# Optimization experiments

Measured on AMD Instinct MI355X. Metric: run time of the kernel, lower is better.

## Reference

```python
import jax, jax.numpy as jnp
import numpy as np

B, T, S, D = 16, 64, 256, 512
NEG_INF = -1e9  # finite stand-in for -inf mask fill (identical sparsemax output, autodiff-safe)


def sparsemax(z, axis=-1):
    # sparsemax(z) = clip(z - tau, 0), tau from sorted cumsum threshold
    z = z - jnp.max(z, axis=axis, keepdims=True)
    z_srt = -jnp.sort(-z, axis=axis)                      # descending sort
    z_cum = jnp.cumsum(z_srt, axis=axis) - 1.0
    k = jnp.arange(1, z.shape[axis] + 1, dtype=z.dtype)   # rho = 1..d
    support = (k * z_srt) > z_cum
    supp_size = jnp.sum(support, axis=axis, keepdims=True)
    tau = jnp.take_along_axis(z_cum, supp_size - 1, axis=axis) / supp_size.astype(z.dtype)
    return jnp.clip(z - tau, 0.0)


def setup_inputs() -> dict:
    key = jax.random.key(0)
    ks = jax.random.split(key, 9)
    init = lambda k, shape: (jax.random.normal(k, shape, jnp.float32) * 0.05)
    return {
        "source": jax.random.normal(ks[0], (B, T, D), jnp.float32),
        "memory_bank": jax.random.normal(ks[1], (B, S, D), jnp.float32),
        "memory_mask": jax.random.randint(ks[2], (B, S), 0, 2).astype(jnp.int32),
        "W_q": init(ks[3], (D, D)),   # linear_query weight
        "b_q": init(ks[4], (D,)),     # linear_query bias
        "W_c": init(ks[5], (D, D)),   # linear_context weight (no bias)
        "v": init(ks[6], (D,)),       # v projection (dim -> 1)
        "W_out": init(ks[7], (D, 2 * D)),  # linear_out weight
        "b_out": init(ks[8], (D,)),        # linear_out bias (mlp path has bias)
    }


def reference(source, memory_bank, memory_mask, W_q, b_q, W_c, v, W_out, b_out):
    # MLP (Bahdanau) score: v^T tanh(W_q q + U_c h)
    wq = jnp.einsum('btd,ed->bte', source, W_q) + b_q        # (B,T,D)
    uh = jnp.einsum('bsd,ed->bse', memory_bank, W_c)         # (B,S,D)
    wquh = jnp.tanh(wq[:, :, None, :] + uh[:, None, :, :])   # (B,T,S,D) big intermediate
    align = jnp.einsum('btsd,d->bts', wquh, v)               # (B,T,S)
    align = jnp.where(memory_mask[:, None, :].astype(bool), align, NEG_INF)
    align_vectors = sparsemax(align, axis=-1)                # (B,T,S)
    c = jnp.einsum('bts,bsd->btd', align_vectors, memory_bank)
    concat_c = jnp.concatenate([c, source], axis=-1)         # (B,T,2D)
    attn_h = jnp.einsum('btf,df->btd', concat_c, W_out) + b_out  # no tanh on mlp path
    return attn_h.transpose(1, 0, 2), align_vectors.transpose(1, 0, 2)
```

## Files before the change

kernel.cpp:

```cpp
#include <hip/hip_runtime.h>
#include <hip/hip_bf16.h>

#define BB 16
#define TT 64
#define SS 256
#define DD 512

typedef __bf16 bf16x8 __attribute__((ext_vector_type(8)));
typedef float f32x4 __attribute__((ext_vector_type(4)));

__device__ __forceinline__ ushort f2b(float x) {
    __hip_bfloat16 h = __float2bfloat16(x);
    return __builtin_bit_cast(ushort, h);
}
__device__ __forceinline__ float b2f(ushort u) {
    unsigned int x = (unsigned int)u << 16;
    return __builtin_bit_cast(float, x);
}

#define S_SRC (BB * TT * DD)
#define S_MB  (BB * SS * DD)
#define S_WQ  (DD * DD)
#define S_WC  (DD * DD)
#define S_WO  (DD * 2 * DD)

__global__ __launch_bounds__(256) void cast_all(
    const float* __restrict__ src, const float* __restrict__ mb,
    const float* __restrict__ wq, const float* __restrict__ wc,
    const float* __restrict__ wo,
    ushort* __restrict__ src_b, ushort* __restrict__ mb_b,
    ushort* __restrict__ wq_b, ushort* __restrict__ wc_b,
    ushort* __restrict__ wo_b) {
    int g = blockIdx.x * 256 + threadIdx.x;
    const int G0 = S_SRC / 4, G1 = S_MB / 4, G2 = S_WQ / 4, G3 = S_WC / 4;
    const float* in;
    ushort* out;
    int local;
    if (g < G0) { in = src; out = src_b; local = g; }
    else if (g < G0 + G1) { in = mb; out = mb_b; local = g - G0; }
    else if (g < G0 + G1 + G2) { in = wq; out = wq_b; local = g - G0 - G1; }
    else if (g < G0 + G1 + G2 + G3) { in = wc; out = wc_b; local = g - G0 - G1 - G2; }
    else { in = wo; out = wo_b; local = g - G0 - G1 - G2 - G3; }
    float4 x = *(const float4*)(in + (size_t)local * 4);
    ushort4 y = {f2b(x.x), f2b(x.y), f2b(x.z), f2b(x.w)};
    *(ushort4*)(out + (size_t)local * 4) = y;
}

__global__ __launch_bounds__(256) void mega_gemm(
    const ushort* __restrict__ src_b, const ushort* __restrict__ mb_b,
    const ushort* __restrict__ wqw_b, const ushort* __restrict__ wcw_b,
    const ushort* __restrict__ wo_b,
    const float* __restrict__ b_q, const float* __restrict__ b_out,
    float* __restrict__ Ewq, float* __restrict__ Y,
    ushort* __restrict__ EuT, ushort* __restrict__ M2) {
    __shared__ ushort Asm[64 * 72];
    __shared__ ushort Bsm[64 * 72];
    const int id = blockIdx.x;
    const ushort* Ab;
    const ushort* Bb;
    const float* bias = nullptr;
    void* Cp;
    int ldb, N, m0, n0;
    bool exp2x, obf16, hasb;
    size_t coff = 0;
    if (id < 256) {
        const bool isY = id >= 128;
        const int l = id & 127;
        m0 = (l >> 3) * 64; n0 = (l & 7) * 64;
        Ab = src_b;
        Bb = isY ? (wo_b + DD) : wqw_b;
        ldb = isY ? 2 * DD : DD;
        bias = isY ? b_out : b_q;
        hasb = true; exp2x = !isY; obf16 = false; N = DD;
        Cp = isY ? (void*)Y : (void*)Ewq;
    } else if (id < 768) {
        const int l = id - 256;
        const int bz = l >> 5, tl = l & 31;
        m0 = (tl >> 2) * 64; n0 = (tl & 3) * 64;
        Ab = wcw_b;
        Bb = mb_b + (size_t)bz * SS * DD;
        ldb = DD;
        hasb = false; exp2x = true; obf16 = true; N = SS;
        Cp = (void*)EuT; coff = (size_t)bz * DD * SS;
    } else {
        const int l = id - 768;
        const int bz = l >> 5, tl = l & 31;
        m0 = (tl >> 3) * 64; n0 = (tl & 7) * 64;
        Ab = mb_b + (size_t)bz * SS * DD;
        Bb = wo_b;
        ldb = 2 * DD;
        hasb = false; exp2x = false; obf16 = true; N = DD;
        Cp = (void*)M2; coff = (size_t)bz * SS * DD;
    }

    const int tid = threadIdx.x;
    const int lane = tid & 63;
    const int wave = tid >> 6;
    const int wm = wave & 1, wn = wave >> 1;

    const int srow = tid >> 3;
    const int schunk = tid & 7;
    const ushort* Ag0 = Ab + (size_t)(m0 + srow) * DD + schunk * 8;
    const ushort* Ag1 = Ag0 + (size_t)32 * DD;
    const ushort* Bg0 = Bb + (size_t)(n0 + srow) * ldb + schunk * 8;
    const ushort* Bg1 = Bg0 + (size_t)32 * ldb;
    const int lw = srow * 72 + schunk * 8;

    const int l15 = lane & 15, quad = lane >> 4;
    const int ar = (wm * 32 + l15) * 72 + quad * 8;
    const int br = (wn * 32 + l15) * 72 + quad * 8;

    f32x4 acc00 = {0.f, 0.f, 0.f, 0.f}, acc01 = {0.f, 0.f, 0.f, 0.f};
    f32x4 acc10 = {0.f, 0.f, 0.f, 0.f}, acc11 = {0.f, 0.f, 0.f, 0.f};

    uint4 a0 = *(const uint4*)Ag0;
    uint4 a1 = *(const uint4*)Ag1;
    uint4 b0 = *(const uint4*)Bg0;
    uint4 b1 = *(const uint4*)Bg1;
    const int P = DD >> 6;
    for (int p = 0; p < P; ++p) {
        __syncthreads();
        *(uint4*)&Asm[lw] = a0;
        *(uint4*)&Asm[lw + 32 * 72] = a1;
        *(uint4*)&Bsm[lw] = b0;
        *(uint4*)&Bsm[lw + 32 * 72] = b1;
        __syncthreads();
        if (p + 1 < P) {
            int ko = (p + 1) << 6;
            a0 = *(const uint4*)(Ag0 + ko);
            a1 = *(const uint4*)(Ag1 + ko);
            b0 = *(const uint4*)(Bg0 + ko);
            b1 = *(const uint4*)(Bg1 + ko);
        }
        bf16x8 fa0 = *(const bf16x8*)&Asm[ar];
        bf16x8 fa1 = *(const bf16x8*)&Asm[ar + 16 * 72];
        bf16x8 fb0 = *(const bf16x8*)&Bsm[br];
        bf16x8 fb1 = *(const bf16x8*)&Bsm[br + 16 * 72];
        acc00 = __builtin_amdgcn_mfma_f32_16x16x32_bf16(fa0, fb0, acc00, 0, 0, 0);
        acc01 = __builtin_amdgcn_mfma_f32_16x16x32_bf16(fa0, fb1, acc01, 0, 0, 0);
        acc10 = __builtin_amdgcn_mfma_f32_16x16x32_bf16(fa1, fb0, acc10, 0, 0, 0);
        acc11 = __builtin_amdgcn_mfma_f32_16x16x32_bf16(fa1, fb1, acc11, 0, 0, 0);
        fa0 = *(const bf16x8*)&Asm[ar + 32];
        fa1 = *(const bf16x8*)&Asm[ar + 16 * 72 + 32];
        fb0 = *(const bf16x8*)&Bsm[br + 32];
        fb1 = *(const bf16x8*)&Bsm[br + 16 * 72 + 32];
        acc00 = __builtin_amdgcn_mfma_f32_16x16x32_bf16(fa0, fb0, acc00, 0, 0, 0);
        acc01 = __builtin_amdgcn_mfma_f32_16x16x32_bf16(fa0, fb1, acc01, 0, 0, 0);
        acc10 = __builtin_amdgcn_mfma_f32_16x16x32_bf16(fa1, fb0, acc10, 0, 0, 0);
        acc11 = __builtin_amdgcn_mfma_f32_16x16x32_bf16(fa1, fb1, acc11, 0, 0, 0);
    }
    const int nA = n0 + wn * 32 + l15;
    float bias0 = 0.f, bias1 = 0.f;
    if (hasb) { bias0 = bias[nA]; bias1 = bias[nA + 16]; }
    float* Cf = (float*)Cp;
    ushort* Cb = (ushort*)Cp;
#pragma unroll
    for (int mt = 0; mt < 2; ++mt) {
        f32x4 accN0 = mt ? acc10 : acc00;
        f32x4 accN1 = mt ? acc11 : acc01;
#pragma unroll
        for (int r = 0; r < 4; ++r) {
            int m = m0 + wm * 32 + mt * 16 + quad * 4 + r;
            float v0 = accN0[r] + bias0;
            float v1 = accN1[r] + bias1;
            if (exp2x) { v0 = __expf(2.0f * v0); v1 = __expf(2.0f * v1); }
            size_t i0 = coff + (size_t)m * N + nA;
            if (obf16) { Cb[i0] = f2b(v0); Cb[i0 + 16] = f2b(v1); }
            else { Cf[i0] = v0; Cf[i0 + 16] = v1; }
        }
    }
}

__global__ __launch_bounds__(256) void align5(const float* __restrict__ Ewq,
                                              const ushort* __restrict__ EuT,
                                              const int* __restrict__ mask,
                                              const float* __restrict__ v,
                                              const ushort* __restrict__ M2,
                                              const float* __restrict__ Y,
                                              float* __restrict__ align_out,
                                              float* __restrict__ out0) {
    const int tg = blockIdx.x, b = blockIdx.y;
    const int t0 = tg * 2, t1 = t0 + 1;
    const int bt0 = b * TT + t0, bt1 = bt0 + 1;
    const int tid = threadIdx.x;
    const int lane = tid & 63;
    const int wave = tid >> 6;
    __shared__ float4 EL[DD];
    __shared__ float zs0[SS], zs1[SS];
    __shared__ float svp[4];
    __shared__ float4 cmb[2][128];
    __shared__ int lst0[SS], lst1[SS];
    __shared__ int cnt[2];

    if (tid < 2) cnt[tid] = 0;
    const float* E0p = Ewq + (size_t)bt0 * DD;
    const float* E1p = Ewq + (size_t)bt1 * DD;
    float pv = 0.f;
    for (int d = tid; d < DD; d += 256) {
        float vv = v[d];
        EL[d] = make_float4(E0p[d], E1p[d], vv, 0.f);
        pv += vv;
    }
#pragma unroll
    for (int off = 32; off > 0; off >>= 1) pv += __shfl_xor(pv, off, 64);
    if (lane == 0) svp[wave] = pv;
    __syncthreads();
    const float sv = svp[0] + svp[1] + svp[2] + svp[3];

    const ushort* U = EuT + (size_t)b * DD * SS + tid;
    float a0 = 0.f, a1 = 0.f;
#pragma unroll 16
    for (int d = 0; d < DD; ++d) {
        float u = b2f(U[(size_t)d * SS]);
        float4 el = EL[d];
        float den0 = __builtin_fmaf(el.x, u, 1.0f);
        float den1 = __builtin_fmaf(el.y, u, 1.0f);
        a0 = __builtin_fmaf(el.z, __builtin_amdgcn_rcpf(den0), a0);
        a1 = __builtin_fmaf(el.z, __builtin_amdgcn_rcpf(den1), a1);
    }
    int mk = mask[b * SS + tid];
    zs0[tid] = mk ? (sv - 2.0f * a0) : -1e9f;
    zs1[tid] = mk ? (sv - 2.0f * a1) : -1e9f;
    __syncthreads();

    if (wave < 2) {
        float* zz = wave ? zs1 : zs0;
        float z0 = zz[lane];
        float z1 = zz[lane + 64];
        float z2 = zz[lane + 128];
        float z3 = zz[lane + 192];
        float mx = fmaxf(fmaxf(z0, z1), fmaxf(z2, z3));
#pragma unroll
        for (int off = 32; off > 0; off >>= 1) mx = fmaxf(mx, __shfl_xor(mx, off, 64));
        z0 -= mx; z1 -= mx; z2 -= mx; z3 -= mx;
        float lo = -1.0f, hi = 0.0f;
        for (int it = 0; it < 24; ++it) {
            float mid = 0.5f * (lo + hi);
            float ssum = fmaxf(z0 - mid, 0.f) + fmaxf(z1 - mid, 0.f) +
                         fmaxf(z2 - mid, 0.f) + fmaxf(z3 - mid, 0.f);
#pragma unroll
            for (int off = 32; off > 0; off >>= 1) ssum += __shfl_xor(ssum, off, 64);
            if (ssum >= 1.0f) lo = mid; else hi = mid;
        }
        float tau = 0.5f * (lo + hi);
        zz[lane] = fmaxf(z0 - tau, 0.f);
        zz[lane + 64] = fmaxf(z1 - tau, 0.f);
        zz[lane + 128] = fmaxf(z2 - tau, 0.f);
        zz[lane + 192] = fmaxf(z3 - tau, 0.f);
    }
    __syncthreads();

    align_out[((size_t)t0 * BB + b) * SS + tid] = zs0[tid];
    align_out[((size_t)t1 * BB + b) * SS + tid] = zs1[tid];

    if (zs0[tid] > 0.f) lst0[atomicAdd(&cnt[0], 1)] = tid;
    if (zs1[tid] > 0.f) lst1[atomicAdd(&cnt[1], 1)] = tid;
    __syncthreads();
    const int n0c = cnt[0], n1c = cnt[1];

    const int ch = tid & 127, sg = tid >> 7;
    const ushort* M2b = M2 + (size_t)b * SS * DD + ch * 4;
    float4 at0 = {0.f, 0.f, 0.f, 0.f}, at1 = {0.f, 0.f, 0.f, 0.f};
#pragma unroll 4
    for (int j = sg; j < n0c; j += 2) {
        int s = lst0[j];
        float p = zs0[s];
        ushort4 m4 = *(const ushort4*)(M2b + (size_t)s * DD);
        at0.x = __builtin_fmaf(p, b2f(m4.x), at0.x);
        at0.y = __builtin_fmaf(p, b2f(m4.y), at0.y);
        at0.z = __builtin_fmaf(p, b2f(m4.z), at0.z);
        at0.w = __builtin_fmaf(p, b2f(m4.w), at0.w);
    }
#pragma unroll 4
    for (int j = sg; j < n1c; j += 2) {
        int s = lst1[j];
        float p = zs1[s];
        ushort4 m4 = *(const ushort4*)(M2b + (size_t)s * DD);
        at1.x = __builtin_fmaf(p, b2f(m4.x), at1.x);
        at1.y = __builtin_fmaf(p, b2f(m4.y), at1.y);
        at1.z = __builtin_fmaf(p, b2f(m4.z), at1.z);
        at1.w = __builtin_fmaf(p, b2f(m4.w), at1.w);
    }
    if (sg == 1) { cmb[0][ch] = at0; cmb[1][ch] = at1; }
    __syncthreads();
    if (sg == 0) {
        float4 p0 = cmb[0][ch], p1 = cmb[1][ch];
        const float4* Y0 = (const float4*)(Y + (size_t)bt0 * DD);
        const float4* Y1 = (const float4*)(Y + (size_t)bt1 * DD);
        float4 y0 = Y0[ch], y1 = Y1[ch];
        float4 o0, o1;
        o0.x = at0.x + p0.x + y0.x; o0.y = at0.y + p0.y + y0.y;
        o0.z = at0.z + p0.z + y0.z; o0.w = at0.w + p0.w + y0.w;
        o1.x = at1.x + p1.x + y1.x; o1.y = at1.y + p1.y + y1.y;
        o1.z = at1.z + p1.z + y1.z; o1.w = at1.w + p1.w + y1.w;
        float4* O0 = (float4*)(out0 + ((size_t)t0 * BB + b) * DD);
        float4* O1 = (float4*)(out0 + ((size_t)t1 * BB + b) * DD);
        O0[ch] = o0;
        O1[ch] = o1;
    }
}

extern "C" void kernel_launch(void* const* d_in, const int* in_sizes, int n_in,
                              void* d_out, int out_size, void* d_ws, size_t ws_size,
                              hipStream_t stream) {
    const float* source = (const float*)d_in[0];
    const float* memory_bank = (const float*)d_in[1];
    const int* memory_mask = (const int*)d_in[2];
    const float* W_q = (const float*)d_in[3];
    const float* b_q = (const float*)d_in[4];
    const float* W_c = (const float*)d_in[5];
    const float* v = (const float*)d_in[6];
    const float* W_out = (const float*)d_in[7];
    const float* b_out = (const float*)d_in[8];

    float* out0 = (float*)d_out;
    float* out1 = out0 + (size_t)TT * BB * DD;

    float* Ewq = (float*)d_ws;
    float* Y = Ewq + S_SRC;
    ushort* EuT = (ushort*)(Y + S_SRC);
    ushort* M2 = EuT + S_MB;
    ushort* src_b = M2 + S_MB;
    ushort* mb_b = src_b + S_SRC;
    ushort* wqw_b = mb_b + S_MB;
    ushort* wcw_b = wqw_b + S_WQ;
    ushort* wo_b = wcw_b + S_WC;

    dim3 blk(256);
    int ngroups = (S_SRC + S_MB + S_WQ + S_WC + S_WO) / 4;
    cast_all<<<dim3(ngroups / 256), blk, 0, stream>>>(
        source, memory_bank, W_q, W_c, W_out, src_b, mb_b, wqw_b, wcw_b, wo_b);
    mega_gemm<<<dim3(1280), blk, 0, stream>>>(
        src_b, mb_b, wqw_b, wcw_b, wo_b, b_q, b_out, Ewq, Y, EuT, M2);
    align5<<<dim3(TT / 2, BB), blk, 0, stream>>>(
        Ewq, EuT, memory_mask, v, M2, Y, out1, out0);
}
```

Baseline: 125.4 us.

## Fuse fp32-to-bf16 cast into GEMM loads and double-buffer shared memory

Removes the separate cast_all kernel. The GEMM now reads fp32 inputs directly and packs them to bf16 while writing them into shared memory. This drops one launch and the write and re-read of the bf16 copies. The shared-memory tiles are also double-buffered so there is one barrier per k-step instead of two, and the launch bound requests 4 blocks per CU. In exchange, each GEMM tile reads twice the bytes from global memory, and memory_bank and the weights are re-read in fp32 by many blocks. Register pressure also rises from holding eight float4 prefetch registers.

```diff
diff --git a/kernel.cpp b/kernel.cpp
--- a/kernel.cpp
+++ b/kernel.cpp
@@ -17,47 +17,27 @@
     unsigned int x = (unsigned int)u << 16;
     return __builtin_bit_cast(float, x);
 }
-
-#define S_SRC (BB * TT * DD)
-#define S_MB  (BB * SS * DD)
-#define S_WQ  (DD * DD)
-#define S_WC  (DD * DD)
-#define S_WO  (DD * 2 * DD)
-
-__global__ __launch_bounds__(256) void cast_all(
+__device__ __forceinline__ uint4 pack8(float4 lo, float4 hi) {
+    uint4 r;
+    r.x = (unsigned)f2b(lo.x) | ((unsigned)f2b(lo.y) << 16);
+    r.y = (unsigned)f2b(lo.z) | ((unsigned)f2b(lo.w) << 16);
+    r.z = (unsigned)f2b(hi.x) | ((unsigned)f2b(hi.y) << 16);
+    r.w = (unsigned)f2b(hi.z) | ((unsigned)f2b(hi.w) << 16);
+    return r;
+}
+
+__global__ __launch_bounds__(256, 4) void mega_gemm(
     const float* __restrict__ src, const float* __restrict__ mb,
     const float* __restrict__ wq, const float* __restrict__ wc,
     const float* __restrict__ wo,
-    ushort* __restrict__ src_b, ushort* __restrict__ mb_b,
-    ushort* __restrict__ wq_b, ushort* __restrict__ wc_b,
-    ushort* __restrict__ wo_b) {
-    int g = blockIdx.x * 256 + threadIdx.x;
-    const int G0 = S_SRC / 4, G1 = S_MB / 4, G2 = S_WQ / 4, G3 = S_WC / 4;
-    const float* in;
-    ushort* out;
-    int local;
-    if (g < G0) { in = src; out = src_b; local = g; }
-    else if (g < G0 + G1) { in = mb; out = mb_b; local = g - G0; }
-    else if (g < G0 + G1 + G2) { in = wq; out = wq_b; local = g - G0 - G1; }
-    else if (g < G0 + G1 + G2 + G3) { in = wc; out = wc_b; local = g - G0 - G1 - G2; }
-    else { in = wo; out = wo_b; local = g - G0 - G1 - G2 - G3; }
-    float4 x = *(const float4*)(in + (size_t)local * 4);
-    ushort4 y = {f2b(x.x), f2b(x.y), f2b(x.z), f2b(x.w)};
-    *(ushort4*)(out + (size_t)local * 4) = y;
-}
-
-__global__ __launch_bounds__(256) void mega_gemm(
-    const ushort* __restrict__ src_b, const ushort* __restrict__ mb_b,
-    const ushort* __restrict__ wqw_b, const ushort* __restrict__ wcw_b,
-    const ushort* __restrict__ wo_b,
     const float* __restrict__ b_q, const float* __restrict__ b_out,
     float* __restrict__ Ewq, float* __restrict__ Y,
     ushort* __restrict__ EuT, ushort* __restrict__ M2) {
-    __shared__ ushort Asm[64 * 72];
-    __shared__ ushort Bsm[64 * 72];
+    __shared__ ushort Asm[2][64 * 72];
+    __shared__ ushort Bsm[2][64 * 72];
     const int id = blockIdx.x;
-    const ushort* Ab;
-    const ushort* Bb;
+    const float* Ab;
+    const float* Bb;
     const float* bias = nullptr;
     void* Cp;
     int ldb, N, m0, n0;
@@ -67,8 +47,8 @@
         const bool isY = id >= 128;
         const int l = id & 127;
         m0 = (l >> 3) * 64; n0 = (l & 7) * 64;
-        Ab = src_b;
-        Bb = isY ? (wo_b + DD) : wqw_b;
+        Ab = src;
+        Bb = isY ? (wo + DD) : wq;
         ldb = isY ? 2 * DD : DD;
         bias = isY ? b_out : b_q;
         hasb = true; exp2x = !isY; obf16 = false; N = DD;
@@ -77,8 +57,8 @@
         const int l = id - 256;
         const int bz = l >> 5, tl = l & 31;
         m0 = (tl >> 2) * 64; n0 = (tl & 3) * 64;
-        Ab = wcw_b;
-        Bb = mb_b + (size_t)bz * SS * DD;
+        Ab = wc;
+        Bb = mb + (size_t)bz * SS * DD;
         ldb = DD;
         hasb = false; exp2x = true; obf16 = true; N = SS;
         Cp = (void*)EuT; coff = (size_t)bz * DD * SS;
@@ -86,8 +66,8 @@
         const int l = id - 768;
         const int bz = l >> 5, tl = l & 31;
         m0 = (tl >> 3) * 64; n0 = (tl & 7) * 64;
-        Ab = mb_b + (size_t)bz * SS * DD;
-        Bb = wo_b;
+        Ab = mb + (size_t)bz * SS * DD;
+        Bb = wo;
         ldb = 2 * DD;
         hasb = false; exp2x = false; obf16 = true; N = DD;
         Cp = (void*)M2; coff = (size_t)bz * SS * DD;
@@ -100,10 +80,10 @@
 
     const int srow = tid >> 3;
     const int schunk = tid & 7;
-    const ushort* Ag0 = Ab + (size_t)(m0 + srow) * DD + schunk * 8;
-    const ushort* Ag1 = Ag0 + (size_t)32 * DD;
-    const ushort* Bg0 = Bb + (size_t)(n0 + srow) * ldb + schunk * 8;
-    const ushort* Bg1 = Bg0 + (size_t)32 * ldb;
+    const float* Ag0 = Ab + (size_t)(m0 + srow) * DD + schunk * 8;
+    const float* Ag1 = Ag0 + (size_t)32 * DD;
+    const float* Bg0 = Bb + (size_t)(n0 + srow) * ldb + schunk * 8;
+    const float* Bg1 = Bg0 + (size_t)32 * ldb;
     const int lw = srow * 72 + schunk * 8;
 
     const int l15 = lane & 15, quad = lane >> 4;
@@ -113,42 +93,55 @@
     f32x4 acc00 = {0.f, 0.f, 0.f, 0.f}, acc01 = {0.f, 0.f, 0.f, 0.f};
     f32x4 acc10 = {0.f, 0.f, 0.f, 0.f}, acc11 = {0.f, 0.f, 0.f, 0.f};
 
-    uint4 a0 = *(const uint4*)Ag0;
-    uint4 a1 = *(const uint4*)Ag1;
-    uint4 b0 = *(const uint4*)Bg0;
-    uint4 b1 = *(const uint4*)Bg1;
+    float4 a0l, a0h, a1l, a1h, b0l, b0h, b1l, b1h;
+#define LOAD8(ko)                                        \
+    a0l = *(const float4*)(Ag0 + (ko));                  \
+    a0h = *(const float4*)(Ag0 + (ko) + 4);              \
+    a1l = *(const float4*)(Ag1 + (ko));                  \
+    a1h = *(const float4*)(Ag1 + (ko) + 4);              \
+    b0l = *(const float4*)(Bg0 + (ko));                  \
+    b0h = *(const float4*)(Bg0 + (ko) + 4);              \
+    b1l = *(const float4*)(Bg1 + (ko));                  \
+    b1h = *(const float4*)(Bg1 + (ko) + 4);
+#define STORE8(bufi)                                     \
+    *(uint4*)&Asm[bufi][lw] = pack8(a0l, a0h);           \
+    *(uint4*)&Asm[bufi][lw + 32 * 72] = pack8(a1l, a1h); \
+    *(uint4*)&Bsm[bufi][lw] = pack8(b0l, b0h);           \
+    *(uint4*)&Bsm[bufi][lw + 32 * 72] = pack8(b1l, b1h);
+
     const int P = DD >> 6;
+    LOAD8(0)
+    STORE8(0)
+    LOAD8(64)
+    __syncthreads();
+#pragma unroll 2
     for (int p = 0; p < P; ++p) {
-        __syncthreads();
-        *(uint4*)&Asm[lw] = a0;
-        *(uint4*)&Asm[lw + 32 * 72] = a1;
-        *(uint4*)&Bsm[lw] = b0;
-        *(uint4*)&Bsm[lw + 32 * 72] = b1;
-        __syncthreads();
-        if (p + 1 < P) {
-            int ko = (p + 1) << 6;
-            a0 = *(const uint4*)(Ag0 + ko);
-            a1 = *(const uint4*)(Ag1 + ko);
-            b0 = *(const uint4*)(Bg0 + ko);
-            b1 = *(const uint4*)(Bg1 + ko);
-        }
-        bf16x8 fa0 = *(const bf16x8*)&Asm[ar];
-        bf16x8 fa1 = *(const bf16x8*)&Asm[ar + 16 * 72];
-        bf16x8 fb0 = *(const bf16x8*)&Bsm[br];
-        bf16x8 fb1 = *(const bf16x8*)&Bsm[br + 16 * 72];
+        const int cb = p & 1, nb = cb ^ 1;
+        bf16x8 fa0 = *(const bf16x8*)&Asm[cb][ar];
+        bf16x8 fa1 = *(const bf16x8*)&Asm[cb][ar + 16 * 72];
+        bf16x8 fb0 = *(const bf16x8*)&Bsm[cb][br];
+        bf16x8 fb1 = *(const bf16x8*)&Bsm[cb][br + 16 * 72];
         acc00 = __builtin_amdgcn_mfma_f32_16x16x32_bf16(fa0, fb0, acc00, 0, 0, 0);
         acc01 = __builtin_amdgcn_mfma_f32_16x16x32_bf16(fa0, fb1, acc01, 0, 0, 0);
         acc10 = __builtin_amdgcn_mfma_f32_16x16x32_bf16(fa1, fb0, acc10, 0, 0, 0);
         acc11 = __builtin_amdgcn_mfma_f32_16x16x32_bf16(fa1, fb1, acc11, 0, 0, 0);
-        fa0 = *(const bf16x8*)&Asm[ar + 32];
-        fa1 = *(const bf16x8*)&Asm[ar + 16 * 72 + 32];
-        fb0 = *(const bf16x8*)&Bsm[br + 32];
-        fb1 = *(const bf16x8*)&Bsm[br + 16 * 72 + 32];
+        fa0 = *(const bf16x8*)&Asm[cb][ar + 32];
+        fa1 = *(const bf16x8*)&Asm[cb][ar + 16 * 72 + 32];
+        fb0 = *(const bf16x8*)&Bsm[cb][br + 32];
+        fb1 = *(const bf16x8*)&Bsm[cb][br + 16 * 72 + 32];
         acc00 = __builtin_amdgcn_mfma_f32_16x16x32_bf16(fa0, fb0, acc00, 0, 0, 0);
         acc01 = __builtin_amdgcn_mfma_f32_16x16x32_bf16(fa0, fb1, acc01, 0, 0, 0);
         acc10 = __builtin_amdgcn_mfma_f32_16x16x32_bf16(fa1, fb0, acc10, 0, 0, 0);
         acc11 = __builtin_amdgcn_mfma_f32_16x16x32_bf16(fa1, fb1, acc11, 0, 0, 0);
-    }
+        if (p + 1 < P) {
+            STORE8(nb)
+            if (p + 2 < P) { LOAD8((p + 2) << 6) }
+        }
+        __syncthreads();
+    }
+#undef LOAD8
+#undef STORE8
+
     const int nA = n0 + wn * 32 + l15;
     float bias0 = 0.f, bias1 = 0.f;
     if (hasb) { bias0 = bias[nA]; bias1 = bias[nA + 16]; }
@@ -300,6 +293,9 @@
     }
 }
 
+#define S_SRC (BB * TT * DD)
+#define S_MB  (BB * SS * DD)
+
 extern "C" void kernel_launch(void* const* d_in, const int* in_sizes, int n_in,
                               void* d_out, int out_size, void* d_ws, size_t ws_size,
                               hipStream_t stream) {
@@ -320,18 +316,10 @@
     float* Y = Ewq + S_SRC;
     ushort* EuT = (ushort*)(Y + S_SRC);
     ushort* M2 = EuT + S_MB;
-    ushort* src_b = M2 + S_MB;
-    ushort* mb_b = src_b + S_SRC;
-    ushort* wqw_b = mb_b + S_MB;
-    ushort* wcw_b = wqw_b + S_WQ;
-    ushort* wo_b = wcw_b + S_WC;
 
     dim3 blk(256);
-    int ngroups = (S_SRC + S_MB + S_WQ + S_WC + S_WO) / 4;
-    cast_all<<<dim3(ngroups / 256), blk, 0, stream>>>(
-        source, memory_bank, W_q, W_c, W_out, src_b, mb_b, wqw_b, wcw_b, wo_b);
     mega_gemm<<<dim3(1280), blk, 0, stream>>>(
-        src_b, mb_b, wqw_b, wcw_b, wo_b, b_q, b_out, Ewq, Y, EuT, M2);
+        source, memory_bank, W_q, W_c, W_out, b_q, b_out, Ewq, Y, EuT, M2);
     align5<<<dim3(TT / 2, BB), blk, 0, stream>>>(
         Ewq, EuT, memory_mask, v, M2, Y, out1, out0);
 }
```

New measurement: 128.8 us. +2.7%, slower.
